# Performance work log

Hardware: AMD Instinct MI355X
Metric: run time of the kernel (lower is better)

## Reference

```python
import jax, jax.numpy as jnp
import numpy as np

NUM_HEADS = 16
NUM_KV_HEADS = 4
HEAD_DIM = 64
HIDDEN = 1024
R_SOFTPLUS_0 = 1.442695041


def setup_inputs() -> dict:
    key = jax.random.key(0)
    ks = jax.random.split(key, 6)
    B, S = 2, 2048
    qkv_out = (NUM_HEADS + 2 * NUM_KV_HEADS) * HEAD_DIM  # 1536
    return {
        "hidden_states": jax.random.normal(ks[0], (B, S, HIDDEN), dtype=jnp.float32),
        "scaling": jax.random.normal(ks[1], (HEAD_DIM,), dtype=jnp.float32),
        "qkv_w": jax.random.normal(ks[2], (qkv_out, HIDDEN), dtype=jnp.float32) * (1.0 / np.sqrt(HIDDEN)),
        "qkv_b": jax.random.normal(ks[3], (qkv_out,), dtype=jnp.float32) * 0.01,
        "o_w": jax.random.normal(ks[4], (HIDDEN, NUM_HEADS * HEAD_DIM), dtype=jnp.float32) * (1.0 / np.sqrt(NUM_HEADS * HEAD_DIM)),
        "o_b": jax.random.normal(ks[5], (HIDDEN,), dtype=jnp.float32) * 0.01,
    }


def reference(hidden_states, scaling, qkv_w, qkv_b, o_w, o_b):
    B, S, _ = hidden_states.shape
    H, KV, D = NUM_HEADS, NUM_KV_HEADS, HEAD_DIM
    rep = H // KV

    qkv = hidden_states @ qkv_w.T + qkv_b  # [B,S,(H+2KV)*D]
    xq, xk, xv = jnp.split(qkv, [H * D, H * D + KV * D], axis=-1)
    xq = xq.reshape(B, S, H, D)
    xk = xk.reshape(B, S, KV, D)
    xv = xv.reshape(B, S, KV, D)

    # per-dim softplus scaling of queries
    scale = (R_SOFTPLUS_0 / jnp.sqrt(jnp.float32(D))) * jax.nn.softplus(scaling)
    xq = xq * scale[None, None, None, :]

    # GQA: repeat kv heads to match query heads
    xk = jnp.repeat(xk, rep, axis=2)  # [B,S,H,D]
    xv = jnp.repeat(xv, rep, axis=2)

    scores = jnp.einsum("bqhd,bkhd->bhqk", xq, xk)  # [B,H,S,S]
    probs = jax.nn.softmax(scores.astype(jnp.float32), axis=-1).astype(xq.dtype)
    out = jnp.einsum("bhqk,bkhd->bqhd", probs, xv)  # [B,S,H,D]
    out = out.reshape(B, S, H * D)
    return out @ o_w.T + o_b
```

## Files before the change

kernel.cpp:

```cpp
#include <hip/hip_runtime.h>
#include <stdint.h>

#define HQ 16
#define HKV 4
#define DH 64
#define HID 1024
#define QKVN 1536
#define SEQ 2048
#define NB 2
#define NTOK 4096

typedef __bf16 bf16x8 __attribute__((ext_vector_type(8)));
typedef __bf16 bf16x2 __attribute__((ext_vector_type(2)));
typedef float f32x4 __attribute__((ext_vector_type(4)));
typedef float f32x16 __attribute__((ext_vector_type(16)));
typedef unsigned int u32;
typedef unsigned short u16;

__device__ __forceinline__ u32 pk(float lo, float hi) {
  bf16x2 t;
  t[0] = (__bf16)lo;
  t[1] = (__bf16)hi;
  return __builtin_bit_cast(u32, t);
}
__device__ __forceinline__ u16 bf1(float f) {
  return __builtin_bit_cast(u16, (__bf16)f);
}

__device__ __forceinline__ void gl_lds16(const void* g, void* l) {
  __builtin_amdgcn_global_load_lds(
      (__attribute__((address_space(1))) u32*)(uintptr_t)g,
      (__attribute__((address_space(3))) u32*)(u32)(uintptr_t)l, 16, 0, 0);
}

#if __has_builtin(__builtin_amdgcn_exp2f)
#define EXP2(x) __builtin_amdgcn_exp2f(x)
#else
#define EXP2(x) __expf((x) * 0.69314718055994531f)
#endif

#if __has_builtin(__builtin_amdgcn_fdot2_f32_bf16)
#define HAVE_DOT2 1
#endif

#define FENCE() asm volatile("" ::: "memory")

__global__ void cvt_bf16_kernel(const float* __restrict__ h,
                                const float* __restrict__ w1,
                                const float* __restrict__ w2,
                                u16* __restrict__ oh, u16* __restrict__ ow1,
                                u16* __restrict__ ow2) {
  const int NH = NTOK * HID / 8, NW1 = QKVN * HID / 8, NW2 = HID * HID / 8;
  int idx = blockIdx.x * blockDim.x + threadIdx.x;
  if (idx >= NH + NW1 + NW2) return;
  const float* s; u16* d; int o;
  if (idx < NH) { s = h; d = oh; o = idx; }
  else if (idx < NH + NW1) { s = w1; d = ow1; o = idx - NH; }
  else { s = w2; d = ow2; o = idx - NH - NW1; }
  const float4* sp = (const float4*)s + (size_t)o * 2;
  float4 a = sp[0], b = sp[1];
  uint4 out;
  out.x = pk(a.x, a.y);
  out.y = pk(a.z, a.w);
  out.z = pk(b.x, b.y);
  out.w = pk(b.z, b.w);
  *((uint4*)(d + (size_t)o * 8)) = out;
}

template <int EPI>
__global__ __launch_bounds__(256, 3) void gemm_nt_kernel(
    const u16* __restrict__ A, const u16* __restrict__ Bw,
    const float* __restrict__ bias, const float* __restrict__ scaling,
    void* __restrict__ Out, int ldout, u16* __restrict__ vt) {
  constexpr int BM = 64;
  constexpr int MR = BM / 32;
  constexpr int ACH = BM / 32;
  constexpr int BUF = BM * 128 + 16384;
  __shared__ char smem[2 * BUF];
  const int tid = threadIdx.x;
  const int lane = tid & 63, wid = tid >> 6;
  const int l15 = lane & 15, lg = lane >> 4;
  const int wr = wid >> 1, wc = wid & 1;
  const int mt = blockIdx.x * BM, nt = blockIdx.y * 128;

  const u16* ag[ACH]; const u16* bg[4]; int al[ACH]; int bl[4];
#pragma unroll
  for (int c = 0; c < ACH; c++) {
    int chunk = wid * ACH + c;
    int rp = chunk * 8 + (lane >> 3);
    int lb = (lane & 7) ^ (rp & 7);
    ag[c] = A + (size_t)(mt + rp) * HID + lb * 8;
    al[c] = chunk * 1024;
  }
#pragma unroll
  for (int c = 0; c < 4; c++) {
    int chunk = wid * 4 + c;
    int rp = chunk * 8 + (lane >> 3);
    int lb = (lane & 7) ^ (rp & 7);
    bg[c] = Bw + (size_t)(nt + rp) * HID + lb * 8;
    bl[c] = BM * 128 + chunk * 1024;
  }

  f32x4 acc[MR][4] = {};

#pragma unroll
  for (int c = 0; c < ACH; c++) gl_lds16(ag[c], smem + al[c]);
#pragma unroll
  for (int c = 0; c < 4; c++) gl_lds16(bg[c], smem + bl[c]);

  for (int kt = 0; kt < HID / 64; kt++) {
    const int cur = (kt & 1) * BUF;
    const int nxt = BUF - cur;
    if (kt < HID / 64 - 1) {
#pragma unroll
      for (int c = 0; c < ACH; c++) gl_lds16(ag[c] + (kt + 1) * 64, smem + nxt + al[c]);
#pragma unroll
      for (int c = 0; c < 4; c++) gl_lds16(bg[c] + (kt + 1) * 64, smem + nxt + bl[c]);
      asm volatile("s_waitcnt vmcnt(6)" ::: "memory");
    } else {
      asm volatile("s_waitcnt vmcnt(0)" ::: "memory");
    }
    __builtin_amdgcn_s_barrier();
    FENCE();
    const char* Asm = smem + cur;
    const char* Bsm = smem + cur + BM * 128;
#pragma unroll
    for (int kk = 0; kk < 2; kk++) {
      bf16x8 af[MR], bfr[4];
#pragma unroll
      for (int mi = 0; mi < MR; mi++) {
        int row = wr * (BM / 2) + mi * 16 + l15;
        int blk = kk * 4 + lg;
        af[mi] = *(const bf16x8*)(Asm + row * 128 + ((blk ^ (row & 7)) << 4));
      }
#pragma unroll
      for (int nj = 0; nj < 4; nj++) {
        int row = wc * 64 + nj * 16 + l15;
        int blk = kk * 4 + lg;
        bfr[nj] = *(const bf16x8*)(Bsm + row * 128 + ((blk ^ (row & 7)) << 4));
      }
#pragma unroll
      for (int mi = 0; mi < MR; mi++)
#pragma unroll
        for (int nj = 0; nj < 4; nj++)
          acc[mi][nj] = __builtin_amdgcn_mfma_f32_16x16x32_bf16(af[mi], bfr[nj],
                                                                acc[mi][nj], 0, 0, 0);
    }
    asm volatile("s_waitcnt lgkmcnt(0)" ::: "memory");
    __builtin_amdgcn_sched_barrier(0);
    __builtin_amdgcn_s_barrier();
    FENCE();
  }

  if (EPI == 0) {
    float qs[4];
#pragma unroll
    for (int nj = 0; nj < 4; nj++) {
      int col = nt + wc * 64 + nj * 16 + l15;
      if (col < HQ * DH) {
        float x = scaling[col & 63];
        float sp = (x > 15.f) ? x : log1pf(__expf(x));
        qs[nj] = (1.442695041f / 8.0f) * sp * 1.442695041f;
      } else {
        qs[nj] = 1.0f;
      }
    }
    u16* O = (u16*)Out;
#pragma unroll
    for (int mi = 0; mi < MR; mi++)
#pragma unroll
      for (int nj = 0; nj < 4; nj++)
#pragma unroll
        for (int r = 0; r < 4; r++) {
          int row = mt + wr * (BM / 2) + mi * 16 + lg * 4 + r;
          int col = nt + wc * 64 + nj * 16 + l15;
          float v = (acc[mi][nj][r] + bias[col]) * qs[nj];
          O[(size_t)row * ldout + col] = bf1(v);
        }
    if (nt >= (HQ + HKV) * DH) {
#pragma unroll
      for (int mi = 0; mi < MR; mi++)
#pragma unroll
        for (int nj = 0; nj < 4; nj++)
#pragma unroll
          for (int r = 0; r < 4; r++) {
            int row = mt + wr * (BM / 2) + mi * 16 + lg * 4 + r;
            int col = nt + wc * 64 + nj * 16 + l15;
            int vc = col - (HQ + HKV) * DH;
            int kv = vc >> 6, d = vc & 63;
            int b = row >> 11, tok = row & (SEQ - 1);
            float v = acc[mi][nj][r] + bias[col];
            vt[((size_t)(b * HKV + kv) * DH + d) * SEQ + tok] = bf1(v);
          }
    }
  } else {
    float* O = (float*)Out;
#pragma unroll
    for (int mi = 0; mi < MR; mi++)
#pragma unroll
      for (int nj = 0; nj < 4; nj++)
#pragma unroll
        for (int r = 0; r < 4; r++) {
          int row = mt + wr * (BM / 2) + mi * 16 + lg * 4 + r;
          int col = nt + wc * 64 + nj * 16 + l15;
          O[(size_t)row * ldout + col] = acc[mi][nj][r] + bias[col];
        }
  }
}

__global__ __launch_bounds__(512, 4) void attn_kernel(const u16* __restrict__ qkv,
                                                      const u16* __restrict__ vtb,
                                                      u16* __restrict__ aout) {
  __shared__ char smem[65536];
  const int tid = threadIdx.x, lane = tid & 63, wid = tid >> 6;
  const int l31 = lane & 31, hi = lane >> 5;
  const int g = wid >> 2, wg = wid & 3;
  const int kvb = g * 1024;
  const int qt = blockIdx.x, bh = blockIdx.y;
  const int b = bh >> 4, h = bh & 15, kvh = h >> 2;
  const int tb = b * SEQ;
  const int NT = 32;

  bf16x8 qb[4];
  const int qrow_g = tb + qt * 128 + wg * 32 + l31;
#pragma unroll
  for (int kk = 0; kk < 4; kk++)
    qb[kk] = *(const bf16x8*)(qkv + (size_t)qrow_g * QKVN + h * DH + kk * 16 + hi * 8);

  const u16* kg; const u16* vg; int klo, vlo;
  {
    int krow = wg * 8 + (lane >> 3);
    int kd = ((lane & 7) ^ (krow & 7)) * 8;
    int ktok = (krow & ~12) | ((krow & 4) << 1) | ((krow & 8) >> 1);
    kg = qkv + (size_t)(tb + kvb + ktok) * QKVN + HQ * DH + kvh * DH + kd;
    klo = g * 8192 + wg * 1024;
    int vR = wg * 8 + (lane >> 3);
    int vp = (lane & 7) ^ (vR & 7);
    int vd = 2 * vR + (vp >> 2);
    int vgb = vp & 3;
    vg = vtb + (size_t)((b * HKV + kvh) * DH + vd) * SEQ + kvb + vgb * 8;
    vlo = g * 8192 + 4096 + wg * 1024;
  }

  f32x16 ot0 = {}, ot1 = {};
  float l_run = 0.f;

#pragma unroll
  for (int t = 0; t < 2; t++) {
    gl_lds16(kg, smem + t * 16384 + klo);
    gl_lds16(vg, smem + t * 16384 + vlo);
    kg += 32 * QKVN;
    vg += 32;
  }

  const int kswz = l31 & 7;

  for (int kt = 0; kt < NT; kt++) {
    if (kt + 2 < NT) {
      const int stb = ((kt + 2) & 3) * 16384;
      gl_lds16(kg, smem + stb + klo);
      gl_lds16(vg, smem + stb + vlo);
      kg += 32 * QKVN;
      vg += 32;
      asm volatile("s_waitcnt vmcnt(4)" ::: "memory");
    } else if (kt + 1 < NT) {
      asm volatile("s_waitcnt vmcnt(2)" ::: "memory");
    } else {
      asm volatile("s_waitcnt vmcnt(0)" ::: "memory");
    }
    __builtin_amdgcn_s_barrier();
    FENCE();

    const char* Ks = smem + (kt & 3) * 16384 + g * 8192;
    const char* Vs = Ks + 4096;

    f32x16 s = {};
#pragma unroll
    for (int kk = 0; kk < 4; kk++) {
      bf16x8 ka = *(const bf16x8*)(Ks + l31 * 128 + (((kk * 2 + hi) ^ kswz) << 4));
      s = __builtin_amdgcn_mfma_f32_32x32x16_bf16(ka, qb[kk], s, 0, 0, 0);
    }

#pragma unroll
    for (int i = 0; i < 16; i++) s[i] = EXP2(s[i]);

    float lsum = 0.f;
#ifdef HAVE_DOT2
    const bf16x2 ones2 = {(__bf16)1.0f, (__bf16)1.0f};
#else
#pragma unroll
    for (int i = 0; i < 16; i++) lsum += s[i];
#endif
#pragma unroll
    for (int kb = 0; kb < 2; kb++) {
      const int vsw = ((l31 & 1) * 4 + kb * 2 + hi) ^ ((l31 >> 1) & 7);
      bf16x8 va0 = *(const bf16x8*)(Vs + (l31 >> 1) * 128 + (vsw << 4));
      bf16x8 va1 = *(const bf16x8*)(Vs + (16 + (l31 >> 1)) * 128 + (vsw << 4));
      union { u32 u[4]; bf16x8 v; } pa;
#pragma unroll
      for (int w = 0; w < 4; w++)
        pa.u[w] = pk(s[kb * 8 + 2 * w], s[kb * 8 + 2 * w + 1]);
#ifdef HAVE_DOT2
#pragma unroll
      for (int w = 0; w < 4; w++)
        lsum = __builtin_amdgcn_fdot2_f32_bf16(__builtin_bit_cast(bf16x2, pa.u[w]),
                                               ones2, lsum, false);
#endif
      ot0 = __builtin_amdgcn_mfma_f32_32x32x16_bf16(va0, pa.v, ot0, 0, 0, 0);
      ot1 = __builtin_amdgcn_mfma_f32_32x32x16_bf16(va1, pa.v, ot1, 0, 0, 0);
    }
    l_run += lsum + __shfl_xor(lsum, 32);
    asm volatile("s_waitcnt lgkmcnt(0)" ::: "memory");
    __builtin_amdgcn_sched_barrier(0);
    __builtin_amdgcn_s_barrier();
    FENCE();
  }

  __syncthreads();
  if (wid >= 4) {
    int idx = tid - 256;
    float* ex0 = (float*)smem;
    float* ex1 = (float*)(smem + 16384);
#pragma unroll
    for (int j = 0; j < 16; j++) ex0[j * 256 + idx] = ot0[j];
#pragma unroll
    for (int j = 0; j < 16; j++) ex1[j * 256 + idx] = ot1[j];
    ((float*)(smem + 32768))[idx] = l_run;
  }
  __syncthreads();
  if (wid < 4) {
    const float* ex0 = (const float*)smem;
    const float* ex1 = (const float*)(smem + 16384);
    l_run += ((const float*)(smem + 32768))[tid];
#pragma unroll
    for (int j = 0; j < 16; j++) ot0[j] += ex0[j * 256 + tid];
#pragma unroll
    for (int j = 0; j < 16; j++) ot1[j] += ex1[j * 256 + tid];
  }
  __syncthreads();

  u16* Ot = (u16*)smem;
  if (wid < 4) {
    float inv = 1.0f / l_run;
    const int qrow_l = wid * 32 + l31;
#pragma unroll
    for (int dt = 0; dt < 2; dt++)
#pragma unroll
      for (int rq = 0; rq < 4; rq++) {
        int d0 = dt * 32 + rq * 8 + 4 * hi;
        float v0, v1, v2, v3;
        if (dt == 0) {
          v0 = ot0[rq * 4 + 0]; v1 = ot0[rq * 4 + 1]; v2 = ot0[rq * 4 + 2]; v3 = ot0[rq * 4 + 3];
        } else {
          v0 = ot1[rq * 4 + 0]; v1 = ot1[rq * 4 + 1]; v2 = ot1[rq * 4 + 2]; v3 = ot1[rq * 4 + 3];
        }
        u32 wa = pk(v0 * inv, v1 * inv);
        u32 wb = pk(v2 * inv, v3 * inv);
        int ga = ((d0 >> 3) ^ (qrow_l & 7));
        *(u32*)((char*)Ot + qrow_l * 128 + ga * 16 + ((d0 & 7) << 1)) = wa;
        *(u32*)((char*)Ot + qrow_l * 128 + ga * 16 + (((d0 + 2) & 7) << 1)) = wb;
      }
  }
  __syncthreads();
#pragma unroll
  for (int it = 0; it < 2; it++) {
    int gidx = it * 512 + tid;
    int row = gidx >> 3, c8 = gidx & 7;
    int pos = c8 ^ (row & 7);
    uint4 val = *(const uint4*)((const char*)Ot + row * 128 + pos * 16);
    *(uint4*)(aout + (size_t)(tb + qt * 128 + row) * (HQ * DH) + h * DH + c8 * 8) = val;
  }
}

extern "C" void kernel_launch(void* const* d_in, const int* in_sizes, int n_in,
                              void* d_out, int out_size, void* d_ws, size_t ws_size,
                              hipStream_t stream) {
  const float* hs = (const float*)d_in[0];
  const float* scaling = (const float*)d_in[1];
  const float* qkv_w = (const float*)d_in[2];
  const float* qkv_b = (const float*)d_in[3];
  const float* o_w = (const float*)d_in[4];
  const float* o_b = (const float*)d_in[5];
  float* out = (float*)d_out;

  char* ws = (char*)d_ws;
  u16* h_bf = (u16*)ws;
  u16* w1_bf = (u16*)(ws + 8388608);
  u16* w2_bf = (u16*)(ws + 11534336);
  u16* qkv = (u16*)(ws + 13631488);
  u16* vtb = (u16*)(ws + 26214400);
  u16* att = (u16*)(ws + 28311552);

  {
    int tot = (NTOK * HID + QKVN * HID + HID * HID) / 8;
    cvt_bf16_kernel<<<(tot + 255) / 256, 256, 0, stream>>>(hs, qkv_w, o_w, h_bf, w1_bf, w2_bf);
  }
  gemm_nt_kernel<0><<<dim3(NTOK / 64, QKVN / 128), 256, 0, stream>>>(
      h_bf, w1_bf, qkv_b, scaling, qkv, QKVN, vtb);
  attn_kernel<<<dim3(SEQ / 128, NB * HQ), 512, 0, stream>>>(qkv, vtb, att);
  gemm_nt_kernel<1><<<dim3(NTOK / 64, HID / 128), 256, 0, stream>>>(
      att, w2_bf, o_b, nullptr, out, HID, nullptr);
}
```

Before: 83.96 us.

## Load K/V tiles directly from global into registers instead of LDS staging

The attention loop stops staging K and V tiles through a 4-deep LDS ring buffer with async global-to-LDS copies and block barriers. Each wave now loads its K fragments and pre-transposed V fragments straight from global memory into registers every iteration. LDS shrinks to 36 KB by splitting the cross-group reduction of the two output accumulators into two sequential phases. This removes per-iteration barriers and LDS traffic and may raise occupancy, but loses load prefetching and cross-wave sharing. Latency now falls on uncoalesced global or L2 reads.

Measured after the change: 159.5 us. 1.9x slower.

```diff
diff --git a/kernel.cpp b/kernel.cpp
--- a/kernel.cpp
+++ b/kernel.cpp
@@ -211,7 +211,7 @@
 __global__ __launch_bounds__(512, 4) void attn_kernel(const u16* __restrict__ qkv,
                                                       const u16* __restrict__ vtb,
                                                       u16* __restrict__ aout) {
-  __shared__ char smem[65536];
+  __shared__ char smem[36864];
   const int tid = threadIdx.x, lane = tid & 63, wid = tid >> 6;
   const int l31 = lane & 31, hi = lane >> 5;
   const int g = wid >> 2, wg = wid & 3;
@@ -227,59 +227,32 @@
   for (int kk = 0; kk < 4; kk++)
     qb[kk] = *(const bf16x8*)(qkv + (size_t)qrow_g * QKVN + h * DH + kk * 16 + hi * 8);
 
-  const u16* kg; const u16* vg; int klo, vlo;
-  {
-    int krow = wg * 8 + (lane >> 3);
-    int kd = ((lane & 7) ^ (krow & 7)) * 8;
-    int ktok = (krow & ~12) | ((krow & 4) << 1) | ((krow & 8) >> 1);
-    kg = qkv + (size_t)(tb + kvb + ktok) * QKVN + HQ * DH + kvh * DH + kd;
-    klo = g * 8192 + wg * 1024;
-    int vR = wg * 8 + (lane >> 3);
-    int vp = (lane & 7) ^ (vR & 7);
-    int vd = 2 * vR + (vp >> 2);
-    int vgb = vp & 3;
-    vg = vtb + (size_t)((b * HKV + kvh) * DH + vd) * SEQ + kvb + vgb * 8;
-    vlo = g * 8192 + 4096 + wg * 1024;
-  }
+  const int ktok = (l31 & ~12) | ((l31 & 4) << 1) | ((l31 & 8) >> 1);
+  const u16* kp = qkv + (size_t)(tb + kvb + ktok) * QKVN + HQ * DH + kvh * DH + hi * 8;
+  const u16* vp0 = vtb + ((size_t)((b * HKV + kvh) * DH) + l31) * SEQ + kvb + hi * 8;
+  const u16* vp1 = vp0 + (size_t)32 * SEQ;
 
   f32x16 ot0 = {}, ot1 = {};
   float l_run = 0.f;
 
-#pragma unroll
-  for (int t = 0; t < 2; t++) {
-    gl_lds16(kg, smem + t * 16384 + klo);
-    gl_lds16(vg, smem + t * 16384 + vlo);
-    kg += 32 * QKVN;
-    vg += 32;
-  }
-
-  const int kswz = l31 & 7;
-
   for (int kt = 0; kt < NT; kt++) {
-    if (kt + 2 < NT) {
-      const int stb = ((kt + 2) & 3) * 16384;
-      gl_lds16(kg, smem + stb + klo);
-      gl_lds16(vg, smem + stb + vlo);
-      kg += 32 * QKVN;
-      vg += 32;
-      asm volatile("s_waitcnt vmcnt(4)" ::: "memory");
-    } else if (kt + 1 < NT) {
-      asm volatile("s_waitcnt vmcnt(2)" ::: "memory");
-    } else {
-      asm volatile("s_waitcnt vmcnt(0)" ::: "memory");
-    }
-    __builtin_amdgcn_s_barrier();
-    FENCE();
-
-    const char* Ks = smem + (kt & 3) * 16384 + g * 8192;
-    const char* Vs = Ks + 4096;
+    bf16x8 ka0 = *(const bf16x8*)(kp + 0 * 16);
+    bf16x8 ka1 = *(const bf16x8*)(kp + 1 * 16);
+    bf16x8 ka2 = *(const bf16x8*)(kp + 2 * 16);
+    bf16x8 ka3 = *(const bf16x8*)(kp + 3 * 16);
+    bf16x8 va00 = *(const bf16x8*)(vp0 + 0);
+    bf16x8 va01 = *(const bf16x8*)(vp0 + 16);
+    bf16x8 va10 = *(const bf16x8*)(vp1 + 0);
+    bf16x8 va11 = *(const bf16x8*)(vp1 + 16);
+    kp += 32 * QKVN;
+    vp0 += 32;
+    vp1 += 32;
 
     f32x16 s = {};
-#pragma unroll
-    for (int kk = 0; kk < 4; kk++) {
-      bf16x8 ka = *(const bf16x8*)(Ks + l31 * 128 + (((kk * 2 + hi) ^ kswz) << 4));
-      s = __builtin_amdgcn_mfma_f32_32x32x16_bf16(ka, qb[kk], s, 0, 0, 0);
-    }
+    s = __builtin_amdgcn_mfma_f32_32x32x16_bf16(ka0, qb[0], s, 0, 0, 0);
+    s = __builtin_amdgcn_mfma_f32_32x32x16_bf16(ka1, qb[1], s, 0, 0, 0);
+    s = __builtin_amdgcn_mfma_f32_32x32x16_bf16(ka2, qb[2], s, 0, 0, 0);
+    s = __builtin_amdgcn_mfma_f32_32x32x16_bf16(ka3, qb[3], s, 0, 0, 0);
 
 #pragma unroll
     for (int i = 0; i < 16; i++) s[i] = EXP2(s[i]);
@@ -293,9 +266,6 @@
 #endif
 #pragma unroll
     for (int kb = 0; kb < 2; kb++) {
-      const int vsw = ((l31 & 1) * 4 + kb * 2 + hi) ^ ((l31 >> 1) & 7);
-      bf16x8 va0 = *(const bf16x8*)(Vs + (l31 >> 1) * 128 + (vsw << 4));
-      bf16x8 va1 = *(const bf16x8*)(Vs + (16 + (l31 >> 1)) * 128 + (vsw << 4));
       union { u32 u[4]; bf16x8 v; } pa;
 #pragma unroll
       for (int w = 0; w < 4; w++)
@@ -306,34 +276,37 @@
         lsum = __builtin_amdgcn_fdot2_f32_bf16(__builtin_bit_cast(bf16x2, pa.u[w]),
                                                ones2, lsum, false);
 #endif
-      ot0 = __builtin_amdgcn_mfma_f32_32x32x16_bf16(va0, pa.v, ot0, 0, 0, 0);
-      ot1 = __builtin_amdgcn_mfma_f32_32x32x16_bf16(va1, pa.v, ot1, 0, 0, 0);
+      ot0 = __builtin_amdgcn_mfma_f32_32x32x16_bf16(kb ? va01 : va00, pa.v, ot0, 0, 0, 0);
+      ot1 = __builtin_amdgcn_mfma_f32_32x32x16_bf16(kb ? va11 : va10, pa.v, ot1, 0, 0, 0);
     }
     l_run += lsum + __shfl_xor(lsum, 32);
-    asm volatile("s_waitcnt lgkmcnt(0)" ::: "memory");
-    __builtin_amdgcn_sched_barrier(0);
-    __builtin_amdgcn_s_barrier();
-    FENCE();
   }
 
   __syncthreads();
   if (wid >= 4) {
     int idx = tid - 256;
     float* ex0 = (float*)smem;
-    float* ex1 = (float*)(smem + 16384);
 #pragma unroll
     for (int j = 0; j < 16; j++) ex0[j * 256 + idx] = ot0[j];
-#pragma unroll
-    for (int j = 0; j < 16; j++) ex1[j * 256 + idx] = ot1[j];
     ((float*)(smem + 32768))[idx] = l_run;
   }
   __syncthreads();
   if (wid < 4) {
     const float* ex0 = (const float*)smem;
-    const float* ex1 = (const float*)(smem + 16384);
     l_run += ((const float*)(smem + 32768))[tid];
 #pragma unroll
     for (int j = 0; j < 16; j++) ot0[j] += ex0[j * 256 + tid];
+  }
+  __syncthreads();
+  if (wid >= 4) {
+    int idx = tid - 256;
+    float* ex1 = (float*)smem;
+#pragma unroll
+    for (int j = 0; j < 16; j++) ex1[j * 256 + idx] = ot1[j];
+  }
+  __syncthreads();
+  if (wid < 4) {
+    const float* ex1 = (const float*)smem;
 #pragma unroll
     for (int j = 0; j < 16; j++) ot1[j] += ex1[j * 256 + tid];
   }
```
